# Kernel tuning notes

Measured on AMD Instinct MI355X. Metric: run time of the kernel, lower is better.

## Reference

```python
import jax, jax.numpy as jnp
import numpy as np

B, M, SV, OV, R, L, V, E = 256, 10, 32, 32, 128, 12, 1000, 64
M2 = M * M
STATE_DIM = (SV + 1) * M2  # 3300
OBJ_DIM = OV * M2          # 3200


def setup_inputs() -> dict:
    key = jax.random.key(0)
    ks = jax.random.split(key, 24)
    s = 0.02
    inp = {
        "state": jax.random.randint(ks[0], (B, M2), 0, SV),
        "obj": jax.random.randint(ks[1], (B, M2), 0, OV),
        "text": jax.random.randint(ks[2], (B, L), 0, V),
        # state MLP [STATE_DIM,128,128,R]
        "Ws1": jax.random.normal(ks[3], (STATE_DIM, 128)) * s,
        "bs1": jnp.zeros((128,)),
        "Ws2": jax.random.normal(ks[4], (128, 128)) * s,
        "bs2": jnp.zeros((128,)),
        "Ws3": jax.random.normal(ks[5], (128, R)) * s,
        "bs3": jnp.zeros((R,)),
        # object MLP [OBJ_DIM,128,128,R]
        "Wo1": jax.random.normal(ks[6], (OBJ_DIM, 128)) * s,
        "bo1": jnp.zeros((128,)),
        "Wo2": jax.random.normal(ks[7], (128, 128)) * s,
        "bo2": jnp.zeros((128,)),
        "Wo3": jax.random.normal(ks[8], (128, R)) * s,
        "bo3": jnp.zeros((R,)),
        # LSTM text encoder: embedding + single-layer LSTM with hidden=R
        "emb": jax.random.normal(ks[9], (V, E)) * s,
        "Wih": jax.random.normal(ks[10], (E, 4 * R)) * s,
        "Whh": jax.random.normal(ks[11], (R, 4 * R)) * s,
        "b_lstm": jnp.zeros((4 * R,)),
    }
    return inp


def _mlp(x, W1, b1, W2, b2, W3, b3):
    h = jax.nn.relu(x @ W1 + b1)
    h = jax.nn.relu(h @ W2 + b2)
    return h @ W3 + b3


def _lstm_last_hidden(text, emb, Wih, Whh, b):
    # text: (B, L) ids -> final hidden (B, R)
    x = emb[text]                      # (B, L, E)
    xs = jnp.swapaxes(x, 0, 1)         # (L, B, E)
    h0 = jnp.zeros((text.shape[0], R), x.dtype)
    c0 = jnp.zeros((text.shape[0], R), x.dtype)

    def step(carry, xt):
        h, c = carry
        g = xt @ Wih + h @ Whh + b     # (B, 4R)
        i, f, gg, o = jnp.split(g, 4, axis=-1)
        c = jax.nn.sigmoid(f) * c + jax.nn.sigmoid(i) * jnp.tanh(gg)
        h = jax.nn.sigmoid(o) * jnp.tanh(c)
        return (h, c), None

    (h, _), _ = jax.lax.scan(step, (h0, c0), xs)
    return h


def reference(state, obj, text, Ws1, bs1, Ws2, bs2, Ws3, bs3,
              Wo1, bo1, Wo2, bo2, Wo3, bo3, emb, Wih, Whh, b_lstm):
    b = state.shape[0]
    # one-hot encodings (torch scatter_ over channel dim)
    state_oh = jax.nn.one_hot(state, SV, dtype=jnp.float32)   # (B, 100, SV)
    obj_oh = jax.nn.one_hot(obj, OV, dtype=jnp.float32)       # (B, 100, OV)

    # repeat each map map_dim^2 times; copy p gets a one-hot of agent position p
    pos = jnp.eye(M2, dtype=jnp.float32)[None, :, :, None]    # (1, 100 copies, 100 cells, 1)
    state_rep = jnp.broadcast_to(state_oh[:, None], (b, M2, M2, SV))
    state_inp = jnp.concatenate(
        [state_rep, jnp.broadcast_to(pos, (b, M2, M2, 1))], axis=-1
    ).reshape(b * M2, STATE_DIM)
    obj_inp = jnp.broadcast_to(obj_oh[:, None], (b, M2, M2, OV)).reshape(b * M2, OBJ_DIM)

    state_out = _mlp(state_inp, Ws1, bs1, Ws2, bs2, Ws3, bs3)   # (B*100, R)
    object_out = _mlp(obj_inp, Wo1, bo1, Wo2, bo2, Wo3, bo3)    # (B*100, R)

    # text is identical across the 100 copies -> encode once, broadcast
    h = _lstm_last_hidden(text, emb, Wih, Whh, b_lstm)          # (B, R)
    lstm_out = jnp.broadcast_to(h[:, None], (b, M2, R)).reshape(b * M2, R)

    values = state_out * object_out * lstm_out                 # (B*100, R)
    map_pred = values.sum(1).reshape(b, M, M)
    return map_pred
```

## Files before the change

kernel.cpp:

```cpp
#include <hip/hip_runtime.h>


#define B_   256
#define M2_  100
#define R_   128
#define L_   12
#define E_   64
#define NT   1024

typedef _Float16 half2v __attribute__((ext_vector_type(2)));
typedef _Float16 f16x8  __attribute__((ext_vector_type(8)));
typedef float    f32x4  __attribute__((ext_vector_type(4)));

__device__ __forceinline__ float sigf(float x) { return 1.f / (1.f + expf(-x)); }

__device__ __forceinline__ uint pk16(float a, float b) {
    half2v h; h.x = (_Float16)a; h.y = (_Float16)b;
    return __builtin_bit_cast(uint, h);
}

__global__ __launch_bounds__(256) void pack_kernel(
    const float* __restrict__ Whh, const float* __restrict__ Wih,
    const float* __restrict__ Ws2, void* __restrict__ wsv)
{
    _Float16* WhhT = (_Float16*)wsv;
    _Float16* WihT = WhhT + 65536;
    uint*     W2P  = (uint*)(WihT + 32768);
    int g = blockIdx.x * 256 + threadIdx.x;
    if (g < 65536) {
        int r = g >> 9, c = g & 511;
        WhhT[c * 128 + r] = (_Float16)Whh[r * 512 + c];
    } else if (g < 65536 + 32768) {
        int g2 = g - 65536;
        int e = g2 >> 9, c = g2 & 511;
        WihT[c * 64 + e] = (_Float16)Wih[e * 512 + c];
    } else if (g < 65536 + 32768 + 8192) {
        int g3 = g - 65536 - 32768;
        int jp = g3 >> 7, kk = g3 & 127;
        W2P[g3] = pk16(Ws2[(2 * jp) * R_ + kk], Ws2[(2 * jp + 1) * R_ + kk]);
    }
}

__global__ __launch_bounds__(NT) __attribute__((amdgpu_waves_per_eu(4, 4)))
void uvfa_kernel(
    const int* __restrict__ state, const int* __restrict__ obj, const int* __restrict__ text,
    const float* __restrict__ Ws1, const float* __restrict__ bs1,
    const float* __restrict__ bs2, const float* __restrict__ Ws3, const float* __restrict__ bs3,
    const float* __restrict__ Wo1, const float* __restrict__ bo1,
    const float* __restrict__ Wo2, const float* __restrict__ bo2,
    const float* __restrict__ Wo3, const float* __restrict__ bo3,
    const float* __restrict__ emb, const float* __restrict__ b_lstm,
    const _Float16* __restrict__ WhhT, const _Float16* __restrict__ WihT,
    const uint* __restrict__ W2P,
    float* __restrict__ out)
{
    const int b   = blockIdx.x;
    const int tid = threadIdx.x;

    __shared__ __align__(16) uint  U[16064];
    __shared__ __align__(16) float part[NT];
    __shared__ __align__(16) float hbuf[R_];
    __shared__ __align__(16) uint  hpair[R_ / 2];
    __shared__ __align__(16) float tmp[R_], tmp2[R_], wbuf[R_], ubuf[R_], bsbuf[R_];
    __shared__ float redw2[2][112];
    __shared__ int   idx_o[M2_], idx_s[M2_], tids[L_];
    __shared__ float c0s;

    float* xw   = (float*)U;
    float* xemb = (float*)(U + 8192);

    const int lane = tid & 63;
    const int wv   = tid >> 6;
    const int m16  = lane & 15;
    const int kgrp = lane >> 4;

    f16x8 af[2][4];
    #pragma unroll
    for (int tt = 0; tt < 2; ++tt) {
        int col = (2 * wv + tt) * 16 + m16;
        #pragma unroll
        for (int s = 0; s < 4; ++s)
            af[tt][s] = *(const f16x8*)&WhhT[col * 128 + s * 32 + kgrp * 8];
    }

    if (tid < M2_) idx_o[tid] = obj[b * M2_ + tid];
    else if (tid >= 128 && tid < 128 + M2_) idx_s[tid - 128] = state[b * M2_ + tid - 128];
    else if (tid >= 256 && tid < 256 + L_) tids[tid - 256] = text[b * L_ + tid - 256];
    else if (tid >= 384 && tid < 448) hpair[tid - 384] = 0u;
    __syncthreads();
    if (tid < L_ * E_) xemb[(tid >> 6) * 66 + (tid & 63)] = emb[tids[tid >> 6] * E_ + (tid & 63)];
    else if (tid < L_ * E_ + 264) ((float*)(U + 8192 + 792))[tid - L_ * E_] = 0.f;
    __syncthreads();

    {
        f16x8 ax[2];
        #pragma unroll
        for (int s = 0; s < 2; ++s) {
            #pragma unroll
            for (int e = 0; e < 8; ++e)
                ax[s][e] = (_Float16)xemb[m16 * 66 + s * 32 + kgrp * 8 + e];
        }
        #pragma unroll
        for (int h = 0; h < 2; ++h) {
            int col = (wv * 2 + h) * 16 + m16;
            float bl = b_lstm[col];
            f32x4 acc = { bl, bl, bl, bl };
            #pragma unroll
            for (int s = 0; s < 2; ++s) {
                f16x8 bx = *(const f16x8*)&WihT[col * 64 + s * 32 + kgrp * 8];
                acc = __builtin_amdgcn_mfma_f32_16x16x32_f16(ax[s], bx, acc, 0, 0, 0);
            }
            if (kgrp < 3) {
                #pragma unroll
                for (int r = 0; r < 4; ++r)
                    xw[(kgrp * 4 + r) * 512 + col] = acc[r];
            }
        }
    }
    __syncthreads();

    float cst = 0.f;
    for (int t = 0; t < L_; ++t) {
        f16x8 bf[4];
        #pragma unroll
        for (int s = 0; s < 4; ++s) {
            uint4 hb = *(const uint4*)&hpair[s * 16 + kgrp * 4];
            bf[s] = __builtin_bit_cast(f16x8, hb);
        }
        #pragma unroll
        for (int tt = 0; tt < 2; ++tt) {
            int colb = (2 * wv + tt) * 16 + kgrp * 4;
            f32x4 acc = *(const f32x4*)&xw[t * 512 + colb];
            #pragma unroll
            for (int s = 0; s < 4; ++s)
                acc = __builtin_amdgcn_mfma_f32_16x16x32_f16(af[tt][s], bf[s], acc, 0, 0, 0);
            if (m16 == 0) {
                part[colb + 0] = acc[0];
                part[colb + 1] = acc[1];
                part[colb + 2] = acc[2];
                part[colb + 3] = acc[3];
            }
        }
        __syncthreads();
        if (tid < R_) {
            float gi = part[tid], gf = part[R_ + tid], gg = part[2 * R_ + tid], go = part[3 * R_ + tid];
            cst = sigf(gf) * cst + sigf(gi) * tanhf(gg);
            float hn = sigf(go) * tanhf(cst);
            hbuf[tid] = hn;
            float hs = __shfl_down(hn, 1, 64);
            if (!(tid & 1)) hpair[tid >> 1] = pk16(hn, hs);
        }
        __syncthreads();
    }

    {
        const uint4* src = (const uint4*)W2P;
        #pragma unroll
        for (int idx = tid; idx < 2048; idx += NT) {
            uint4 v = src[idx];
            int jp = idx >> 5, kq = idx & 31;
            *(uint4*)&U[jp * 132 + kq * 4] = v;
        }
    }

    const int k = tid & 127, qq = tid >> 7;
    {
        float acc = 0.f;
        int c0i = qq * 13, c1i = c0i + 13 < M2_ ? c0i + 13 : M2_;
        for (int c = c0i; c < c1i; ++c)
            acc += Wo1[(c * 32 + idx_o[c]) * R_ + k];
        part[qq * R_ + k] = acc;
    }
    __syncthreads();
    if (tid < R_) {
        float a = bo1[tid];
        #pragma unroll
        for (int q8 = 0; q8 < 8; ++q8) a += part[q8 * R_ + tid];
        tmp[tid] = fmaxf(a, 0.f);
    }
    __syncthreads();
    {
        float s0 = 0.f, s1 = 0.f, s2 = 0.f, s3 = 0.f;
        int j0 = qq * 16;
        #pragma unroll
        for (int j = 0; j < 16; j += 4) {
            s0 = fmaf(tmp[j0 + j + 0], Wo2[(j0 + j + 0) * R_ + k], s0);
            s1 = fmaf(tmp[j0 + j + 1], Wo2[(j0 + j + 1) * R_ + k], s1);
            s2 = fmaf(tmp[j0 + j + 2], Wo2[(j0 + j + 2) * R_ + k], s2);
            s3 = fmaf(tmp[j0 + j + 3], Wo2[(j0 + j + 3) * R_ + k], s3);
        }
        part[qq * R_ + k] = (s0 + s1) + (s2 + s3);
    }
    __syncthreads();
    if (tid < R_) {
        float a = bo2[tid];
        #pragma unroll
        for (int q8 = 0; q8 < 8; ++q8) a += part[q8 * R_ + tid];
        tmp2[tid] = fmaxf(a, 0.f);
    }
    __syncthreads();
    {
        float s0 = 0.f, s1 = 0.f, s2 = 0.f, s3 = 0.f;
        int j0 = qq * 16;
        #pragma unroll
        for (int j = 0; j < 16; j += 4) {
            s0 = fmaf(tmp2[j0 + j + 0], Wo3[(j0 + j + 0) * R_ + k], s0);
            s1 = fmaf(tmp2[j0 + j + 1], Wo3[(j0 + j + 1) * R_ + k], s1);
            s2 = fmaf(tmp2[j0 + j + 2], Wo3[(j0 + j + 2) * R_ + k], s2);
            s3 = fmaf(tmp2[j0 + j + 3], Wo3[(j0 + j + 3) * R_ + k], s3);
        }
        part[qq * R_ + k] = (s0 + s1) + (s2 + s3);
    }
    __syncthreads();
    if (tid < R_) {
        float a = bo3[tid];
        #pragma unroll
        for (int q8 = 0; q8 < 8; ++q8) a += part[q8 * R_ + tid];
        wbuf[tid] = a * hbuf[tid];
    }
    __syncthreads();

    {
        float s0 = 0.f, s1 = 0.f, s2 = 0.f, s3 = 0.f;
        int j0 = qq * 16;
        const float4* w3 = reinterpret_cast<const float4*>(&Ws3[k * R_ + j0]);
        #pragma unroll
        for (int jj = 0; jj < 4; ++jj) {
            float4 v = w3[jj];
            s0 = fmaf(v.x, wbuf[j0 + jj * 4 + 0], s0);
            s1 = fmaf(v.y, wbuf[j0 + jj * 4 + 1], s1);
            s2 = fmaf(v.z, wbuf[j0 + jj * 4 + 2], s2);
            s3 = fmaf(v.w, wbuf[j0 + jj * 4 + 3], s3);
        }
        part[qq * R_ + k] = (s0 + s1) + (s2 + s3);
    }
    if (tid >= 960) {
        int j = tid - 960;
        float s = bs3[j] * wbuf[j] + bs3[j + 64] * wbuf[j + 64];
        s += __shfl_down(s, 32, 64);
        s += __shfl_down(s, 16, 64);
        s += __shfl_down(s, 8, 64);
        s += __shfl_down(s, 4, 64);
        s += __shfl_down(s, 2, 64);
        s += __shfl_down(s, 1, 64);
        if (j == 0) c0s = s;
    }
    __syncthreads();
    if (tid < R_) {
        float a = 0.f;
        #pragma unroll
        for (int q8 = 0; q8 < 8; ++q8) a += part[q8 * R_ + tid];
        ubuf[tid] = a;
    }
    __syncthreads();

    {
        float acc = 0.f;
        int c0i = qq * 13, c1i = c0i + 13 < M2_ ? c0i + 13 : M2_;
        for (int c = c0i; c < c1i; ++c)
            acc += Ws1[(c * 33 + idx_s[c]) * R_ + k];
        part[qq * R_ + k] = acc;
    }
    __syncthreads();
    if (tid < R_) {
        float a = bs1[tid];
        #pragma unroll
        for (int q8 = 0; q8 < 8; ++q8) a += part[q8 * R_ + tid];
        bsbuf[tid] = a;
    }
    __syncthreads();

    #pragma unroll 4
    for (int pass = 0; pass < 13; ++pass) {
        int idx = pass * NT + tid;
        if (idx < M2_ * R_) {
            int j = idx & 127, p = idx >> 7;
            float v = fmaxf(bsbuf[j] + Ws1[(p * 33 + 32) * R_ + j], 0.f);
            float v2 = __shfl_down(v, 1, 64);
            if (!(j & 1)) U[8448 + p * 68 + (j >> 1)] = pk16(v, v2);
        }
    }
    if (tid < 816) U[8448 + 6800 + tid] = 0u;
    __syncthreads();

    if (wv < 14) {
        const int mtile = wv >> 1, nhalf = wv & 1;
        const uint* Ap = U + 8448 + (mtile * 16 + m16) * 68;
        f16x8 A[4];
        #pragma unroll
        for (int s = 0; s < 4; ++s)
            A[s] = __builtin_bit_cast(f16x8, *(const uint4*)&Ap[s * 16 + kgrp * 4]);
        f32x4 acc[4] = { {0,0,0,0}, {0,0,0,0}, {0,0,0,0}, {0,0,0,0} };
        #pragma unroll
        for (int nt = 0; nt < 4; ++nt) {
            int ko = (nhalf * 4 + nt) * 16 + m16;
            #pragma unroll
            for (int s = 0; s < 4; ++s) {
                const uint* Bp = U + (s * 16 + kgrp * 4) * 132 + ko;
                uint4 bv = { Bp[0], Bp[132], Bp[264], Bp[396] };
                acc[nt] = __builtin_amdgcn_mfma_f32_16x16x32_f16(
                    A[s], __builtin_bit_cast(f16x8, bv), acc[nt], 0, 0, 0);
            }
        }
        float vs0 = 0.f, vs1 = 0.f, vs2 = 0.f, vs3 = 0.f;
        #pragma unroll
        for (int nt = 0; nt < 4; ++nt) {
            int ko = (nhalf * 4 + nt) * 16 + m16;
            float bb = bs2[ko], uu = ubuf[ko];
            vs0 = fmaf(fmaxf(acc[nt][0] + bb, 0.f), uu, vs0);
            vs1 = fmaf(fmaxf(acc[nt][1] + bb, 0.f), uu, vs1);
            vs2 = fmaf(fmaxf(acc[nt][2] + bb, 0.f), uu, vs2);
            vs3 = fmaf(fmaxf(acc[nt][3] + bb, 0.f), uu, vs3);
        }
        vs0 += __shfl_xor(vs0, 1, 64); vs0 += __shfl_xor(vs0, 2, 64);
        vs0 += __shfl_xor(vs0, 4, 64); vs0 += __shfl_xor(vs0, 8, 64);
        vs1 += __shfl_xor(vs1, 1, 64); vs1 += __shfl_xor(vs1, 2, 64);
        vs1 += __shfl_xor(vs1, 4, 64); vs1 += __shfl_xor(vs1, 8, 64);
        vs2 += __shfl_xor(vs2, 1, 64); vs2 += __shfl_xor(vs2, 2, 64);
        vs2 += __shfl_xor(vs2, 4, 64); vs2 += __shfl_xor(vs2, 8, 64);
        vs3 += __shfl_xor(vs3, 1, 64); vs3 += __shfl_xor(vs3, 2, 64);
        vs3 += __shfl_xor(vs3, 4, 64); vs3 += __shfl_xor(vs3, 8, 64);
        if (m16 == 0) {
            int pr = mtile * 16 + kgrp * 4;
            redw2[nhalf][pr + 0] = vs0;
            redw2[nhalf][pr + 1] = vs1;
            redw2[nhalf][pr + 2] = vs2;
            redw2[nhalf][pr + 3] = vs3;
        }
    }
    __syncthreads();

    if (tid < M2_)
        out[b * M2_ + tid] = c0s + redw2[0][tid] + redw2[1][tid];
}

extern "C" void kernel_launch(void* const* d_in, const int* in_sizes, int n_in,
                              void* d_out, int out_size, void* d_ws, size_t ws_size,
                              hipStream_t stream) {
    const int*   state  = (const int*)d_in[0];
    const int*   obj    = (const int*)d_in[1];
    const int*   text   = (const int*)d_in[2];
    const float* Ws1    = (const float*)d_in[3];
    const float* bs1    = (const float*)d_in[4];
    const float* Ws2    = (const float*)d_in[5];
    const float* bs2    = (const float*)d_in[6];
    const float* Ws3    = (const float*)d_in[7];
    const float* bs3    = (const float*)d_in[8];
    const float* Wo1    = (const float*)d_in[9];
    const float* bo1    = (const float*)d_in[10];
    const float* Wo2    = (const float*)d_in[11];
    const float* bo2    = (const float*)d_in[12];
    const float* Wo3    = (const float*)d_in[13];
    const float* bo3    = (const float*)d_in[14];
    const float* emb    = (const float*)d_in[15];
    const float* Wih    = (const float*)d_in[16];
    const float* Whh    = (const float*)d_in[17];
    const float* b_lstm = (const float*)d_in[18];
    float* out = (float*)d_out;

    _Float16* WhhT = (_Float16*)d_ws;
    _Float16* WihT = WhhT + 65536;
    uint*     W2P  = (uint*)(WihT + 32768);

    hipLaunchKernelGGL(pack_kernel, dim3(416), dim3(256), 0, stream, Whh, Wih, Ws2, d_ws);
    hipLaunchKernelGGL(uvfa_kernel, dim3(B_), dim3(NT), 0, stream,
                       state, obj, text, Ws1, bs1, bs2, Ws3, bs3,
                       Wo1, bo1, Wo2, bo2, Wo3, bo3, emb, b_lstm,
                       WhhT, WihT, W2P, out);
}
```

Before: 39.85 us.

## Split fused kernel into parallel LSTM/object/state-sum stage and final combine kernel

Splits the single per-batch kernel into two. The first runs 768 blocks: 256 for the LSTM recurrence, 256 for the object MLP and 256 for the state first-layer gather sum, each writing its result to workspace. The second kernel reads those vectors and does the state MLP combine and output. This spreads the serial per-block chain across more blocks and CUs, and the LSTM weight fragments are pinned in registers with an empty asm. In exchange it adds a kernel launch and a workspace round trip through global memory.

```diff
diff --git a/kernel.cpp b/kernel.cpp
--- a/kernel.cpp
+++ b/kernel.cpp
@@ -6,7 +6,6 @@
 #define R_   128
 #define L_   12
 #define E_   64
-#define NT   1024
 
 typedef _Float16 half2v __attribute__((ext_vector_type(2)));
 typedef _Float16 f16x8  __attribute__((ext_vector_type(8)));
@@ -18,6 +17,8 @@
     half2v h; h.x = (_Float16)a; h.y = (_Float16)b;
     return __builtin_bit_cast(uint, h);
 }
+
+#define PINU4(v) asm volatile("" : "+v"(v.x), "+v"(v.y), "+v"(v.z), "+v"(v.w));
 
 __global__ __launch_bounds__(256) void pack_kernel(
     const float* __restrict__ Whh, const float* __restrict__ Wih,
@@ -41,182 +42,233 @@
     }
 }
 
-__global__ __launch_bounds__(NT) __attribute__((amdgpu_waves_per_eu(4, 4)))
-void uvfa_kernel(
+__global__ __launch_bounds__(1024) __attribute__((amdgpu_waves_per_eu(4, 4)))
+void k1_kernel(
     const int* __restrict__ state, const int* __restrict__ obj, const int* __restrict__ text,
     const float* __restrict__ Ws1, const float* __restrict__ bs1,
-    const float* __restrict__ bs2, const float* __restrict__ Ws3, const float* __restrict__ bs3,
     const float* __restrict__ Wo1, const float* __restrict__ bo1,
     const float* __restrict__ Wo2, const float* __restrict__ bo2,
     const float* __restrict__ Wo3, const float* __restrict__ bo3,
     const float* __restrict__ emb, const float* __restrict__ b_lstm,
     const _Float16* __restrict__ WhhT, const _Float16* __restrict__ WihT,
+    float* __restrict__ wsH, float* __restrict__ wsO3, float* __restrict__ wsBS)
+{
+    const int tid = threadIdx.x;
+    __shared__ __align__(16) uint  U[9248];
+    __shared__ __align__(16) float part[1024];
+    __shared__ __align__(16) float hbuf[R_];
+    __shared__ __align__(16) uint  hpair[R_ / 2];
+    __shared__ __align__(16) float tmp[R_], tmp2[R_];
+    __shared__ int idx[M2_], tids[L_];
+
+    const int k = tid & 127, qq = tid >> 7;
+
+    if (blockIdx.x < 256) {
+        const int b    = blockIdx.x;
+        const int lane = tid & 63;
+        const int wv   = tid >> 6;
+        const int m16  = lane & 15;
+        const int kgrp = lane >> 4;
+        float* xw   = (float*)U;
+        float* xemb = (float*)(U + 8192);
+
+        uint4 afu[2][4];
+        #pragma unroll
+        for (int tt = 0; tt < 2; ++tt) {
+            int col = (2 * wv + tt) * 16 + m16;
+            #pragma unroll
+            for (int s = 0; s < 4; ++s) {
+                afu[tt][s] = *(const uint4*)&WhhT[col * 128 + s * 32 + kgrp * 8];
+                PINU4(afu[tt][s])
+            }
+        }
+
+        if (tid < L_) tids[tid] = text[b * L_ + tid];
+        if (tid >= 64 && tid < 128) hpair[tid - 64] = 0u;
+        __syncthreads();
+        if (tid < L_ * E_) xemb[(tid >> 6) * 66 + (tid & 63)] = emb[tids[tid >> 6] * E_ + (tid & 63)];
+        else ((float*)(U + 8192 + 792))[tid - L_ * E_] = 0.f;
+        __syncthreads();
+
+        {
+            f16x8 ax[2];
+            #pragma unroll
+            for (int s = 0; s < 2; ++s) {
+                #pragma unroll
+                for (int e = 0; e < 8; ++e)
+                    ax[s][e] = (_Float16)xemb[m16 * 66 + s * 32 + kgrp * 8 + e];
+            }
+            #pragma unroll
+            for (int h = 0; h < 2; ++h) {
+                int col = (wv * 2 + h) * 16 + m16;
+                float bl = b_lstm[col];
+                f32x4 acc = { bl, bl, bl, bl };
+                #pragma unroll
+                for (int s = 0; s < 2; ++s) {
+                    f16x8 bx = *(const f16x8*)&WihT[col * 64 + s * 32 + kgrp * 8];
+                    acc = __builtin_amdgcn_mfma_f32_16x16x32_f16(ax[s], bx, acc, 0, 0, 0);
+                }
+                if (kgrp < 3) {
+                    #pragma unroll
+                    for (int r = 0; r < 4; ++r)
+                        xw[(kgrp * 4 + r) * 512 + col] = acc[r];
+                }
+            }
+        }
+        __syncthreads();
+
+        float cst = 0.f;
+        for (int t = 0; t < L_; ++t) {
+            f16x8 bf[4];
+            #pragma unroll
+            for (int s = 0; s < 4; ++s) {
+                uint4 hb = *(const uint4*)&hpair[s * 16 + kgrp * 4];
+                bf[s] = __builtin_bit_cast(f16x8, hb);
+            }
+            #pragma unroll
+            for (int tt = 0; tt < 2; ++tt) {
+                int colb = (2 * wv + tt) * 16 + kgrp * 4;
+                f32x4 acc = *(const f32x4*)&xw[t * 512 + colb];
+                #pragma unroll
+                for (int s = 0; s < 4; ++s)
+                    acc = __builtin_amdgcn_mfma_f32_16x16x32_f16(
+                        __builtin_bit_cast(f16x8, afu[tt][s]), bf[s], acc, 0, 0, 0);
+                if (m16 == 0) {
+                    part[colb + 0] = acc[0];
+                    part[colb + 1] = acc[1];
+                    part[colb + 2] = acc[2];
+                    part[colb + 3] = acc[3];
+                }
+            }
+            __syncthreads();
+            if (tid < R_) {
+                float gi = part[tid], gf = part[R_ + tid], gg = part[2 * R_ + tid], go = part[3 * R_ + tid];
+                cst = sigf(gf) * cst + sigf(gi) * tanhf(gg);
+                float hn = sigf(go) * tanhf(cst);
+                hbuf[tid] = hn;
+                float hs = __shfl_down(hn, 1, 64);
+                if (!(tid & 1)) hpair[tid >> 1] = pk16(hn, hs);
+            }
+            __syncthreads();
+        }
+        if (tid < R_) wsH[b * R_ + tid] = hbuf[tid];
+
+    } else if (blockIdx.x < 512) {
+        const int b = blockIdx.x - 256;
+        if (tid < M2_) idx[tid] = obj[b * M2_ + tid];
+        __syncthreads();
+        {
+            float acc = 0.f;
+            int c0i = qq * 13, c1i = c0i + 13 < M2_ ? c0i + 13 : M2_;
+            for (int c = c0i; c < c1i; ++c)
+                acc += Wo1[(c * 32 + idx[c]) * R_ + k];
+            part[qq * R_ + k] = acc;
+        }
+        __syncthreads();
+        if (tid < R_) {
+            float a = bo1[tid];
+            #pragma unroll
+            for (int q8 = 0; q8 < 8; ++q8) a += part[q8 * R_ + tid];
+            tmp[tid] = fmaxf(a, 0.f);
+        }
+        __syncthreads();
+        {
+            float s0 = 0.f, s1 = 0.f, s2 = 0.f, s3 = 0.f;
+            int j0 = qq * 16;
+            #pragma unroll
+            for (int j = 0; j < 16; j += 4) {
+                s0 = fmaf(tmp[j0 + j + 0], Wo2[(j0 + j + 0) * R_ + k], s0);
+                s1 = fmaf(tmp[j0 + j + 1], Wo2[(j0 + j + 1) * R_ + k], s1);
+                s2 = fmaf(tmp[j0 + j + 2], Wo2[(j0 + j + 2) * R_ + k], s2);
+                s3 = fmaf(tmp[j0 + j + 3], Wo2[(j0 + j + 3) * R_ + k], s3);
+            }
+            part[qq * R_ + k] = (s0 + s1) + (s2 + s3);
+        }
+        __syncthreads();
+        if (tid < R_) {
+            float a = bo2[tid];
+            #pragma unroll
+            for (int q8 = 0; q8 < 8; ++q8) a += part[q8 * R_ + tid];
+            tmp2[tid] = fmaxf(a, 0.f);
+        }
+        __syncthreads();
+        {
+            float s0 = 0.f, s1 = 0.f, s2 = 0.f, s3 = 0.f;
+            int j0 = qq * 16;
+            #pragma unroll
+            for (int j = 0; j < 16; j += 4) {
+                s0 = fmaf(tmp2[j0 + j + 0], Wo3[(j0 + j + 0) * R_ + k], s0);
+                s1 = fmaf(tmp2[j0 + j + 1], Wo3[(j0 + j + 1) * R_ + k], s1);
+                s2 = fmaf(tmp2[j0 + j + 2], Wo3[(j0 + j + 2) * R_ + k], s2);
+                s3 = fmaf(tmp2[j0 + j + 3], Wo3[(j0 + j + 3) * R_ + k], s3);
+            }
+            part[qq * R_ + k] = (s0 + s1) + (s2 + s3);
+        }
+        __syncthreads();
+        if (tid < R_) {
+            float a = bo3[tid];
+            #pragma unroll
+            for (int q8 = 0; q8 < 8; ++q8) a += part[q8 * R_ + tid];
+            wsO3[b * R_ + tid] = a;
+        }
+
+    } else {
+        const int b = blockIdx.x - 512;
+        if (tid < M2_) idx[tid] = state[b * M2_ + tid];
+        __syncthreads();
+        {
+            float acc = 0.f;
+            int c0i = qq * 13, c1i = c0i + 13 < M2_ ? c0i + 13 : M2_;
+            for (int c = c0i; c < c1i; ++c)
+                acc += Ws1[(c * 33 + idx[c]) * R_ + k];
+            part[qq * R_ + k] = acc;
+        }
+        __syncthreads();
+        if (tid < R_) {
+            float a = bs1[tid];
+            #pragma unroll
+            for (int q8 = 0; q8 < 8; ++q8) a += part[q8 * R_ + tid];
+            wsBS[b * R_ + tid] = a;
+        }
+    }
+}
+
+__global__ __launch_bounds__(1024) __attribute__((amdgpu_waves_per_eu(4, 4)))
+void k2_kernel(
+    const float* __restrict__ Ws1, const float* __restrict__ bs2,
+    const float* __restrict__ Ws3, const float* __restrict__ bs3,
     const uint* __restrict__ W2P,
+    const float* __restrict__ wsH, const float* __restrict__ wsO3,
+    const float* __restrict__ wsBS,
     float* __restrict__ out)
 {
     const int b   = blockIdx.x;
     const int tid = threadIdx.x;
 
     __shared__ __align__(16) uint  U[16064];
-    __shared__ __align__(16) float part[NT];
-    __shared__ __align__(16) float hbuf[R_];
-    __shared__ __align__(16) uint  hpair[R_ / 2];
-    __shared__ __align__(16) float tmp[R_], tmp2[R_], wbuf[R_], ubuf[R_], bsbuf[R_];
+    __shared__ __align__(16) float part[1024];
+    __shared__ __align__(16) float wbuf[R_], ubuf[R_], bsbuf[R_];
     __shared__ float redw2[2][112];
-    __shared__ int   idx_o[M2_], idx_s[M2_], tids[L_];
     __shared__ float c0s;
-
-    float* xw   = (float*)U;
-    float* xemb = (float*)(U + 8192);
 
     const int lane = tid & 63;
     const int wv   = tid >> 6;
     const int m16  = lane & 15;
     const int kgrp = lane >> 4;
-
-    f16x8 af[2][4];
-    #pragma unroll
-    for (int tt = 0; tt < 2; ++tt) {
-        int col = (2 * wv + tt) * 16 + m16;
-        #pragma unroll
-        for (int s = 0; s < 4; ++s)
-            af[tt][s] = *(const f16x8*)&WhhT[col * 128 + s * 32 + kgrp * 8];
-    }
-
-    if (tid < M2_) idx_o[tid] = obj[b * M2_ + tid];
-    else if (tid >= 128 && tid < 128 + M2_) idx_s[tid - 128] = state[b * M2_ + tid - 128];
-    else if (tid >= 256 && tid < 256 + L_) tids[tid - 256] = text[b * L_ + tid - 256];
-    else if (tid >= 384 && tid < 448) hpair[tid - 384] = 0u;
-    __syncthreads();
-    if (tid < L_ * E_) xemb[(tid >> 6) * 66 + (tid & 63)] = emb[tids[tid >> 6] * E_ + (tid & 63)];
-    else if (tid < L_ * E_ + 264) ((float*)(U + 8192 + 792))[tid - L_ * E_] = 0.f;
-    __syncthreads();
-
-    {
-        f16x8 ax[2];
-        #pragma unroll
-        for (int s = 0; s < 2; ++s) {
-            #pragma unroll
-            for (int e = 0; e < 8; ++e)
-                ax[s][e] = (_Float16)xemb[m16 * 66 + s * 32 + kgrp * 8 + e];
-        }
-        #pragma unroll
-        for (int h = 0; h < 2; ++h) {
-            int col = (wv * 2 + h) * 16 + m16;
-            float bl = b_lstm[col];
-            f32x4 acc = { bl, bl, bl, bl };
-            #pragma unroll
-            for (int s = 0; s < 2; ++s) {
-                f16x8 bx = *(const f16x8*)&WihT[col * 64 + s * 32 + kgrp * 8];
-                acc = __builtin_amdgcn_mfma_f32_16x16x32_f16(ax[s], bx, acc, 0, 0, 0);
-            }
-            if (kgrp < 3) {
-                #pragma unroll
-                for (int r = 0; r < 4; ++r)
-                    xw[(kgrp * 4 + r) * 512 + col] = acc[r];
-            }
-        }
-    }
-    __syncthreads();
-
-    float cst = 0.f;
-    for (int t = 0; t < L_; ++t) {
-        f16x8 bf[4];
-        #pragma unroll
-        for (int s = 0; s < 4; ++s) {
-            uint4 hb = *(const uint4*)&hpair[s * 16 + kgrp * 4];
-            bf[s] = __builtin_bit_cast(f16x8, hb);
-        }
-        #pragma unroll
-        for (int tt = 0; tt < 2; ++tt) {
-            int colb = (2 * wv + tt) * 16 + kgrp * 4;
-            f32x4 acc = *(const f32x4*)&xw[t * 512 + colb];
-            #pragma unroll
-            for (int s = 0; s < 4; ++s)
-                acc = __builtin_amdgcn_mfma_f32_16x16x32_f16(af[tt][s], bf[s], acc, 0, 0, 0);
-            if (m16 == 0) {
-                part[colb + 0] = acc[0];
-                part[colb + 1] = acc[1];
-                part[colb + 2] = acc[2];
-                part[colb + 3] = acc[3];
-            }
-        }
-        __syncthreads();
-        if (tid < R_) {
-            float gi = part[tid], gf = part[R_ + tid], gg = part[2 * R_ + tid], go = part[3 * R_ + tid];
-            cst = sigf(gf) * cst + sigf(gi) * tanhf(gg);
-            float hn = sigf(go) * tanhf(cst);
-            hbuf[tid] = hn;
-            float hs = __shfl_down(hn, 1, 64);
-            if (!(tid & 1)) hpair[tid >> 1] = pk16(hn, hs);
-        }
-        __syncthreads();
-    }
-
+    const int k = tid & 127, qq = tid >> 7;
+
+    if (tid < R_) {
+        wbuf[tid]  = wsH[b * R_ + tid] * wsO3[b * R_ + tid];
+        bsbuf[tid] = wsBS[b * R_ + tid];
+    }
     {
         const uint4* src = (const uint4*)W2P;
         #pragma unroll
-        for (int idx = tid; idx < 2048; idx += NT) {
+        for (int idx = tid; idx < 2048; idx += 1024) {
             uint4 v = src[idx];
             int jp = idx >> 5, kq = idx & 31;
             *(uint4*)&U[jp * 132 + kq * 4] = v;
         }
-    }
-
-    const int k = tid & 127, qq = tid >> 7;
-    {
-        float acc = 0.f;
-        int c0i = qq * 13, c1i = c0i + 13 < M2_ ? c0i + 13 : M2_;
-        for (int c = c0i; c < c1i; ++c)
-            acc += Wo1[(c * 32 + idx_o[c]) * R_ + k];
-        part[qq * R_ + k] = acc;
-    }
-    __syncthreads();
-    if (tid < R_) {
-        float a = bo1[tid];
-        #pragma unroll
-        for (int q8 = 0; q8 < 8; ++q8) a += part[q8 * R_ + tid];
-        tmp[tid] = fmaxf(a, 0.f);
-    }
-    __syncthreads();
-    {
-        float s0 = 0.f, s1 = 0.f, s2 = 0.f, s3 = 0.f;
-        int j0 = qq * 16;
-        #pragma unroll
-        for (int j = 0; j < 16; j += 4) {
-            s0 = fmaf(tmp[j0 + j + 0], Wo2[(j0 + j + 0) * R_ + k], s0);
-            s1 = fmaf(tmp[j0 + j + 1], Wo2[(j0 + j + 1) * R_ + k], s1);
-            s2 = fmaf(tmp[j0 + j + 2], Wo2[(j0 + j + 2) * R_ + k], s2);
-            s3 = fmaf(tmp[j0 + j + 3], Wo2[(j0 + j + 3) * R_ + k], s3);
-        }
-        part[qq * R_ + k] = (s0 + s1) + (s2 + s3);
-    }
-    __syncthreads();
-    if (tid < R_) {
-        float a = bo2[tid];
-        #pragma unroll
-        for (int q8 = 0; q8 < 8; ++q8) a += part[q8 * R_ + tid];
-        tmp2[tid] = fmaxf(a, 0.f);
-    }
-    __syncthreads();
-    {
-        float s0 = 0.f, s1 = 0.f, s2 = 0.f, s3 = 0.f;
-        int j0 = qq * 16;
-        #pragma unroll
-        for (int j = 0; j < 16; j += 4) {
-            s0 = fmaf(tmp2[j0 + j + 0], Wo3[(j0 + j + 0) * R_ + k], s0);
-            s1 = fmaf(tmp2[j0 + j + 1], Wo3[(j0 + j + 1) * R_ + k], s1);
-            s2 = fmaf(tmp2[j0 + j + 2], Wo3[(j0 + j + 2) * R_ + k], s2);
-            s3 = fmaf(tmp2[j0 + j + 3], Wo3[(j0 + j + 3) * R_ + k], s3);
-        }
-        part[qq * R_ + k] = (s0 + s1) + (s2 + s3);
-    }
-    __syncthreads();
-    if (tid < R_) {
-        float a = bo3[tid];
-        #pragma unroll
-        for (int q8 = 0; q8 < 8; ++q8) a += part[q8 * R_ + tid];
-        wbuf[tid] = a * hbuf[tid];
     }
     __syncthreads();
 
@@ -245,34 +297,9 @@
         s += __shfl_down(s, 1, 64);
         if (j == 0) c0s = s;
     }
-    __syncthreads();
-    if (tid < R_) {
-        float a = 0.f;
-        #pragma unroll
-        for (int q8 = 0; q8 < 8; ++q8) a += part[q8 * R_ + tid];
-        ubuf[tid] = a;
-    }
-    __syncthreads();
-
-    {
-        float acc = 0.f;
-        int c0i = qq * 13, c1i = c0i + 13 < M2_ ? c0i + 13 : M2_;
-        for (int c = c0i; c < c1i; ++c)
-            acc += Ws1[(c * 33 + idx_s[c]) * R_ + k];
-        part[qq * R_ + k] = acc;
-    }
-    __syncthreads();
-    if (tid < R_) {
-        float a = bs1[tid];
-        #pragma unroll
-        for (int q8 = 0; q8 < 8; ++q8) a += part[q8 * R_ + tid];
-        bsbuf[tid] = a;
-    }
-    __syncthreads();
-
     #pragma unroll 4
     for (int pass = 0; pass < 13; ++pass) {
-        int idx = pass * NT + tid;
+        int idx = pass * 1024 + tid;
         if (idx < M2_ * R_) {
             int j = idx & 127, p = idx >> 7;
             float v = fmaxf(bsbuf[j] + Ws1[(p * 33 + 32) * R_ + j], 0.f);
@@ -281,6 +308,13 @@
         }
     }
     if (tid < 816) U[8448 + 6800 + tid] = 0u;
+    __syncthreads();
+    if (tid < R_) {
+        float a = 0.f;
+        #pragma unroll
+        for (int q8 = 0; q8 < 8; ++q8) a += part[q8 * R_ + tid];
+        ubuf[tid] = a;
+    }
     __syncthreads();
 
     if (wv < 14) {
@@ -361,10 +395,15 @@
     _Float16* WhhT = (_Float16*)d_ws;
     _Float16* WihT = WhhT + 65536;
     uint*     W2P  = (uint*)(WihT + 32768);
+    float*    wsH  = (float*)(W2P + 8192);
+    float*    wsO3 = wsH + 32768;
+    float*    wsBS = wsO3 + 32768;
 
     hipLaunchKernelGGL(pack_kernel, dim3(416), dim3(256), 0, stream, Whh, Wih, Ws2, d_ws);
-    hipLaunchKernelGGL(uvfa_kernel, dim3(B_), dim3(NT), 0, stream,
-                       state, obj, text, Ws1, bs1, bs2, Ws3, bs3,
+    hipLaunchKernelGGL(k1_kernel, dim3(768), dim3(1024), 0, stream,
+                       state, obj, text, Ws1, bs1,
                        Wo1, bo1, Wo2, bo2, Wo3, bo3, emb, b_lstm,
-                       WhhT, WihT, W2P, out);
+                       WhhT, WihT, wsH, wsO3, wsBS);
+    hipLaunchKernelGGL(k2_kernel, dim3(B_), dim3(1024), 0, stream,
+                       Ws1, bs2, Ws3, bs3, W2P, wsH, wsO3, wsBS, out);
 }
```

After: 42.38 us. 1.06x slower.

## Fuse LSTM gate math into MFMA waves and convert MLP weights to fp16

Applied to the files above, without the earlier changes.

The LSTM recurrence now places all four gates for a column in the same wave (8 waves, 4 tiles each), so the gate nonlinearities are computed directly from MFMA accumulators. h is written to a double-buffered shared array, which removes the part-buffer round trip and one barrier per timestep. Separately, the pack kernel now also converts Wo1, Ws1, Wo2, Wo3 and Ws3 to fp16 so the main kernel's gathers and matvecs read half the bytes. The cost is a much larger pack kernel that runs on every call, fp16 rounding of the MLP weights, and register pressure from pinned weight fragments.

```diff
diff --git a/kernel.cpp b/kernel.cpp
--- a/kernel.cpp
+++ b/kernel.cpp
@@ -19,39 +19,57 @@
     return __builtin_bit_cast(uint, h);
 }
 
+#define PINU4(v) asm volatile("" : "+v"(v.x), "+v"(v.y), "+v"(v.z), "+v"(v.w));
+
 __global__ __launch_bounds__(256) void pack_kernel(
     const float* __restrict__ Whh, const float* __restrict__ Wih,
-    const float* __restrict__ Ws2, void* __restrict__ wsv)
+    const float* __restrict__ Ws2, const float* __restrict__ Wo1,
+    const float* __restrict__ Ws1, const float* __restrict__ Wo2,
+    const float* __restrict__ Wo3, const float* __restrict__ Ws3,
+    void* __restrict__ wsv)
 {
     _Float16* WhhT = (_Float16*)wsv;
     _Float16* WihT = WhhT + 65536;
     uint*     W2P  = (uint*)(WihT + 32768);
+    _Float16* Wo1h = (_Float16*)(W2P + 8192);
+    _Float16* Ws1h = Wo1h + 409600;
+    _Float16* Wo2h = Ws1h + 422400;
+    _Float16* Wo3h = Wo2h + 16384;
+    _Float16* Ws3h = Wo3h + 16384;
     int g = blockIdx.x * 256 + threadIdx.x;
     if (g < 65536) {
         int r = g >> 9, c = g & 511;
-        WhhT[c * 128 + r] = (_Float16)Whh[r * 512 + c];
-    } else if (g < 65536 + 32768) {
-        int g2 = g - 65536;
-        int e = g2 >> 9, c = g2 & 511;
-        WihT[c * 64 + e] = (_Float16)Wih[e * 512 + c];
-    } else if (g < 65536 + 32768 + 8192) {
-        int g3 = g - 65536 - 32768;
-        int jp = g3 >> 7, kk = g3 & 127;
+        WhhT[c * 128 + r] = (_Float16)Whh[g];
+    } else if (g < 98304) {
+        int g2 = g - 65536; int e = g2 >> 9, c = g2 & 511;
+        WihT[c * 64 + e] = (_Float16)Wih[g2];
+    } else if (g < 106496) {
+        int g3 = g - 98304; int jp = g3 >> 7, kk = g3 & 127;
         W2P[g3] = pk16(Ws2[(2 * jp) * R_ + kk], Ws2[(2 * jp + 1) * R_ + kk]);
+    } else if (g < 516096) {
+        int i = g - 106496; Wo1h[i] = (_Float16)Wo1[i];
+    } else if (g < 938496) {
+        int i = g - 516096; Ws1h[i] = (_Float16)Ws1[i];
+    } else if (g < 954880) {
+        int i = g - 938496; Wo2h[i] = (_Float16)Wo2[i];
+    } else if (g < 971264) {
+        int i = g - 954880; Wo3h[i] = (_Float16)Wo3[i];
+    } else if (g < 987648) {
+        int i = g - 971264; Ws3h[i] = (_Float16)Ws3[i];
     }
 }
 
 __global__ __launch_bounds__(NT) __attribute__((amdgpu_waves_per_eu(4, 4)))
 void uvfa_kernel(
     const int* __restrict__ state, const int* __restrict__ obj, const int* __restrict__ text,
-    const float* __restrict__ Ws1, const float* __restrict__ bs1,
-    const float* __restrict__ bs2, const float* __restrict__ Ws3, const float* __restrict__ bs3,
-    const float* __restrict__ Wo1, const float* __restrict__ bo1,
-    const float* __restrict__ Wo2, const float* __restrict__ bo2,
-    const float* __restrict__ Wo3, const float* __restrict__ bo3,
+    const float* __restrict__ bs1, const float* __restrict__ bs2, const float* __restrict__ bs3,
+    const float* __restrict__ bo1, const float* __restrict__ bo2, const float* __restrict__ bo3,
     const float* __restrict__ emb, const float* __restrict__ b_lstm,
     const _Float16* __restrict__ WhhT, const _Float16* __restrict__ WihT,
     const uint* __restrict__ W2P,
+    const _Float16* __restrict__ Wo1h, const _Float16* __restrict__ Ws1h,
+    const _Float16* __restrict__ Wo2h, const _Float16* __restrict__ Wo3h,
+    const _Float16* __restrict__ Ws3h,
     float* __restrict__ out)
 {
     const int b   = blockIdx.x;
@@ -60,7 +78,7 @@
     __shared__ __align__(16) uint  U[16064];
     __shared__ __align__(16) float part[NT];
     __shared__ __align__(16) float hbuf[R_];
-    __shared__ __align__(16) uint  hpair[R_ / 2];
+    __shared__ __align__(16) uint  hpair[2][64];
     __shared__ __align__(16) float tmp[R_], tmp2[R_], wbuf[R_], ubuf[R_], bsbuf[R_];
     __shared__ float redw2[2][112];
     __shared__ int   idx_o[M2_], idx_s[M2_], tids[L_];
@@ -73,20 +91,25 @@
     const int wv   = tid >> 6;
     const int m16  = lane & 15;
     const int kgrp = lane >> 4;
-
-    f16x8 af[2][4];
-    #pragma unroll
-    for (int tt = 0; tt < 2; ++tt) {
-        int col = (2 * wv + tt) * 16 + m16;
-        #pragma unroll
-        for (int s = 0; s < 4; ++s)
-            af[tt][s] = *(const f16x8*)&WhhT[col * 128 + s * 32 + kgrp * 8];
+    const int k = tid & 127, qq = tid >> 7;
+
+    uint4 afu[4][4];
+    if (wv < 8) {
+        #pragma unroll
+        for (int g = 0; g < 4; ++g) {
+            int col = (wv + 8 * g) * 16 + m16;
+            #pragma unroll
+            for (int s = 0; s < 4; ++s) {
+                afu[g][s] = *(const uint4*)&WhhT[col * 128 + s * 32 + kgrp * 8];
+                PINU4(afu[g][s])
+            }
+        }
     }
 
     if (tid < M2_) idx_o[tid] = obj[b * M2_ + tid];
     else if (tid >= 128 && tid < 128 + M2_) idx_s[tid - 128] = state[b * M2_ + tid - 128];
     else if (tid >= 256 && tid < 256 + L_) tids[tid - 256] = text[b * L_ + tid - 256];
-    else if (tid >= 384 && tid < 448) hpair[tid - 384] = 0u;
+    else if (tid >= 384 && tid < 448) hpair[0][tid - 384] = 0u;
     __syncthreads();
     if (tid < L_ * E_) xemb[(tid >> 6) * 66 + (tid & 63)] = emb[tids[tid >> 6] * E_ + (tid & 63)];
     else if (tid < L_ * E_ + 264) ((float*)(U + 8192 + 792))[tid - L_ * E_] = 0.f;
@@ -95,11 +118,10 @@
     {
         f16x8 ax[2];
         #pragma unroll
-        for (int s = 0; s < 2; ++s) {
+        for (int s = 0; s < 2; ++s)
             #pragma unroll
             for (int e = 0; e < 8; ++e)
                 ax[s][e] = (_Float16)xemb[m16 * 66 + s * 32 + kgrp * 8 + e];
-        }
         #pragma unroll
         for (int h = 0; h < 2; ++h) {
             int col = (wv * 2 + h) * 16 + m16;
@@ -119,38 +141,46 @@
     }
     __syncthreads();
 
-    float cst = 0.f;
+    float cst0 = 0.f, cst1 = 0.f, cst2 = 0.f, cst3 = 0.f;
+    float h0 = 0.f, h1v = 0.f, h2v = 0.f, h3v = 0.f;
     for (int t = 0; t < L_; ++t) {
-        f16x8 bf[4];
-        #pragma unroll
-        for (int s = 0; s < 4; ++s) {
-            uint4 hb = *(const uint4*)&hpair[s * 16 + kgrp * 4];
-            bf[s] = __builtin_bit_cast(f16x8, hb);
-        }
-        #pragma unroll
-        for (int tt = 0; tt < 2; ++tt) {
-            int colb = (2 * wv + tt) * 16 + kgrp * 4;
-            f32x4 acc = *(const f32x4*)&xw[t * 512 + colb];
+        if (wv < 8) {
+            const uint* hp = hpair[t & 1];
+            f16x8 bf[4];
             #pragma unroll
             for (int s = 0; s < 4; ++s)
-                acc = __builtin_amdgcn_mfma_f32_16x16x32_f16(af[tt][s], bf[s], acc, 0, 0, 0);
+                bf[s] = __builtin_bit_cast(f16x8, *(const uint4*)&hp[s * 16 + kgrp * 4]);
+            f32x4 acc[4];
+            #pragma unroll
+            for (int g = 0; g < 4; ++g) {
+                acc[g] = *(const f32x4*)&xw[t * 512 + (wv + 8 * g) * 16 + kgrp * 4];
+                #pragma unroll
+                for (int s = 0; s < 4; ++s)
+                    acc[g] = __builtin_amdgcn_mfma_f32_16x16x32_f16(
+                        __builtin_bit_cast(f16x8, afu[g][s]), bf[s], acc[g], 0, 0, 0);
+            }
+            cst0 = sigf(acc[1][0]) * cst0 + sigf(acc[0][0]) * tanhf(acc[2][0]);
+            h0   = sigf(acc[3][0]) * tanhf(cst0);
+            cst1 = sigf(acc[1][1]) * cst1 + sigf(acc[0][1]) * tanhf(acc[2][1]);
+            h1v  = sigf(acc[3][1]) * tanhf(cst1);
+            cst2 = sigf(acc[1][2]) * cst2 + sigf(acc[0][2]) * tanhf(acc[2][2]);
+            h2v  = sigf(acc[3][2]) * tanhf(cst2);
+            cst3 = sigf(acc[1][3]) * cst3 + sigf(acc[0][3]) * tanhf(acc[2][3]);
+            h3v  = sigf(acc[3][3]) * tanhf(cst3);
             if (m16 == 0) {
-                part[colb + 0] = acc[0];
-                part[colb + 1] = acc[1];
-                part[colb + 2] = acc[2];
-                part[colb + 3] = acc[3];
+                uint* hw = hpair[(t + 1) & 1];
+                hw[8 * wv + kgrp * 2]     = pk16(h0, h1v);
+                hw[8 * wv + kgrp * 2 + 1] = pk16(h2v, h3v);
             }
         }
         __syncthreads();
-        if (tid < R_) {
-            float gi = part[tid], gf = part[R_ + tid], gg = part[2 * R_ + tid], go = part[3 * R_ + tid];
-            cst = sigf(gf) * cst + sigf(gi) * tanhf(gg);
-            float hn = sigf(go) * tanhf(cst);
-            hbuf[tid] = hn;
-            float hs = __shfl_down(hn, 1, 64);
-            if (!(tid & 1)) hpair[tid >> 1] = pk16(hn, hs);
-        }
-        __syncthreads();
+    }
+    if (wv < 8 && m16 == 0) {
+        int j = wv * 16 + kgrp * 4;
+        hbuf[j + 0] = h0;
+        hbuf[j + 1] = h1v;
+        hbuf[j + 2] = h2v;
+        hbuf[j + 3] = h3v;
     }
 
     {
@@ -163,12 +193,11 @@
         }
     }
 
-    const int k = tid & 127, qq = tid >> 7;
     {
         float acc = 0.f;
         int c0i = qq * 13, c1i = c0i + 13 < M2_ ? c0i + 13 : M2_;
         for (int c = c0i; c < c1i; ++c)
-            acc += Wo1[(c * 32 + idx_o[c]) * R_ + k];
+            acc += (float)Wo1h[(c * 32 + idx_o[c]) * R_ + k];
         part[qq * R_ + k] = acc;
     }
     __syncthreads();
@@ -184,10 +213,10 @@
         int j0 = qq * 16;
         #pragma unroll
         for (int j = 0; j < 16; j += 4) {
-            s0 = fmaf(tmp[j0 + j + 0], Wo2[(j0 + j + 0) * R_ + k], s0);
-            s1 = fmaf(tmp[j0 + j + 1], Wo2[(j0 + j + 1) * R_ + k], s1);
-            s2 = fmaf(tmp[j0 + j + 2], Wo2[(j0 + j + 2) * R_ + k], s2);
-            s3 = fmaf(tmp[j0 + j + 3], Wo2[(j0 + j + 3) * R_ + k], s3);
+            s0 = fmaf(tmp[j0 + j + 0], (float)Wo2h[(j0 + j + 0) * R_ + k], s0);
+            s1 = fmaf(tmp[j0 + j + 1], (float)Wo2h[(j0 + j + 1) * R_ + k], s1);
+            s2 = fmaf(tmp[j0 + j + 2], (float)Wo2h[(j0 + j + 2) * R_ + k], s2);
+            s3 = fmaf(tmp[j0 + j + 3], (float)Wo2h[(j0 + j + 3) * R_ + k], s3);
         }
         part[qq * R_ + k] = (s0 + s1) + (s2 + s3);
     }
@@ -204,10 +233,10 @@
         int j0 = qq * 16;
         #pragma unroll
         for (int j = 0; j < 16; j += 4) {
-            s0 = fmaf(tmp2[j0 + j + 0], Wo3[(j0 + j + 0) * R_ + k], s0);
-            s1 = fmaf(tmp2[j0 + j + 1], Wo3[(j0 + j + 1) * R_ + k], s1);
-            s2 = fmaf(tmp2[j0 + j + 2], Wo3[(j0 + j + 2) * R_ + k], s2);
-            s3 = fmaf(tmp2[j0 + j + 3], Wo3[(j0 + j + 3) * R_ + k], s3);
+            s0 = fmaf(tmp2[j0 + j + 0], (float)Wo3h[(j0 + j + 0) * R_ + k], s0);
+            s1 = fmaf(tmp2[j0 + j + 1], (float)Wo3h[(j0 + j + 1) * R_ + k], s1);
+            s2 = fmaf(tmp2[j0 + j + 2], (float)Wo3h[(j0 + j + 2) * R_ + k], s2);
+            s3 = fmaf(tmp2[j0 + j + 3], (float)Wo3h[(j0 + j + 3) * R_ + k], s3);
         }
         part[qq * R_ + k] = (s0 + s1) + (s2 + s3);
     }
@@ -223,14 +252,21 @@
     {
         float s0 = 0.f, s1 = 0.f, s2 = 0.f, s3 = 0.f;
         int j0 = qq * 16;
-        const float4* w3 = reinterpret_cast<const float4*>(&Ws3[k * R_ + j0]);
-        #pragma unroll
-        for (int jj = 0; jj < 4; ++jj) {
-            float4 v = w3[jj];
-            s0 = fmaf(v.x, wbuf[j0 + jj * 4 + 0], s0);
-            s1 = fmaf(v.y, wbuf[j0 + jj * 4 + 1], s1);
-            s2 = fmaf(v.z, wbuf[j0 + jj * 4 + 2], s2);
-            s3 = fmaf(v.w, wbuf[j0 + jj * 4 + 3], s3);
+        f16x8 va = *(const f16x8*)&Ws3h[k * R_ + j0];
+        f16x8 vb = *(const f16x8*)&Ws3h[k * R_ + j0 + 8];
+        #pragma unroll
+        for (int e = 0; e < 8; e += 4) {
+            s0 = fmaf((float)va[e + 0], wbuf[j0 + e + 0], s0);
+            s1 = fmaf((float)va[e + 1], wbuf[j0 + e + 1], s1);
+            s2 = fmaf((float)va[e + 2], wbuf[j0 + e + 2], s2);
+            s3 = fmaf((float)va[e + 3], wbuf[j0 + e + 3], s3);
+        }
+        #pragma unroll
+        for (int e = 0; e < 8; e += 4) {
+            s0 = fmaf((float)vb[e + 0], wbuf[j0 + 8 + e + 0], s0);
+            s1 = fmaf((float)vb[e + 1], wbuf[j0 + 8 + e + 1], s1);
+            s2 = fmaf((float)vb[e + 2], wbuf[j0 + 8 + e + 2], s2);
+            s3 = fmaf((float)vb[e + 3], wbuf[j0 + 8 + e + 3], s3);
         }
         part[qq * R_ + k] = (s0 + s1) + (s2 + s3);
     }
@@ -258,7 +294,7 @@
         float acc = 0.f;
         int c0i = qq * 13, c1i = c0i + 13 < M2_ ? c0i + 13 : M2_;
         for (int c = c0i; c < c1i; ++c)
-            acc += Ws1[(c * 33 + idx_s[c]) * R_ + k];
+            acc += (float)Ws1h[(c * 33 + idx_s[c]) * R_ + k];
         part[qq * R_ + k] = acc;
     }
     __syncthreads();
@@ -275,7 +311,7 @@
         int idx = pass * NT + tid;
         if (idx < M2_ * R_) {
             int j = idx & 127, p = idx >> 7;
-            float v = fmaxf(bsbuf[j] + Ws1[(p * 33 + 32) * R_ + j], 0.f);
+            float v = fmaxf(bsbuf[j] + (float)Ws1h[(p * 33 + 32) * R_ + j], 0.f);
             float v2 = __shfl_down(v, 1, 64);
             if (!(j & 1)) U[8448 + p * 68 + (j >> 1)] = pk16(v, v2);
         }
@@ -361,10 +397,16 @@
     _Float16* WhhT = (_Float16*)d_ws;
     _Float16* WihT = WhhT + 65536;
     uint*     W2P  = (uint*)(WihT + 32768);
-
-    hipLaunchKernelGGL(pack_kernel, dim3(416), dim3(256), 0, stream, Whh, Wih, Ws2, d_ws);
+    _Float16* Wo1h = (_Float16*)(W2P + 8192);
+    _Float16* Ws1h = Wo1h + 409600;
+    _Float16* Wo2h = Ws1h + 422400;
+    _Float16* Wo3h = Wo2h + 16384;
+    _Float16* Ws3h = Wo3h + 16384;
+
+    hipLaunchKernelGGL(pack_kernel, dim3(3858), dim3(256), 0, stream,
+                       Whh, Wih, Ws2, Wo1, Ws1, Wo2, Wo3, Ws3, d_ws);
     hipLaunchKernelGGL(uvfa_kernel, dim3(B_), dim3(NT), 0, stream,
-                       state, obj, text, Ws1, bs1, bs2, Ws3, bs3,
-                       Wo1, bo1, Wo2, bo2, Wo3, bo3, emb, b_lstm,
-                       WhhT, WihT, W2P, out);
+                       state, obj, text, bs1, bs2, bs3, bo1, bo2, bo3,
+                       emb, b_lstm, WhhT, WihT, W2P,
+                       Wo1h, Ws1h, Wo2h, Wo3h, Ws3h, out);
 }
```

New measurement: 56.09 us. +40.7%, slower.
